# Optimization experiments

Measured on AMD Instinct MI355X. Metric: run time of the kernel, lower is better.

The kernel has to match this reference:

```python
import jax, jax.numpy as jnp
import numpy as np

NH, NW = 5, 5          # attn_neighborhood_size (odd -> symmetric 'same' padding)
HEADS, HEAD_DIM = 8, 64
DIM = 512              # == heads*head_dim, but project_out=True since heads>1
B, HMAP, WMAP = 4, 64, 64
N = HMAP * WMAP


def local_expand(t, height, width):
    """Equivalent of impulse-filter conv2d neighbor gather.

    t: [b, heads, n, d] -> [b, heads, n, NH*NW, d]
    neighbor f=(i,j) of pixel (p,q) is t[p+i-NH//2, q+j-NW//2], zero-padded.
    """
    b, h, n, d = t.shape
    y = t.reshape(b, h, height, width, d)
    ph, pw = NH // 2, NW // 2
    yp = jnp.pad(y, ((0, 0), (0, 0), (ph, ph), (pw, pw), (0, 0)))
    # fixed small loop over the 25 window offsets (row-major = filter order)
    slabs = [yp[:, :, i:i + height, j:j + width, :]
             for i in range(NH) for j in range(NW)]
    out = jnp.stack(slabs, axis=4)  # [b, h, H, W, F, d]
    return out.reshape(b, h, n, NH * NW, d)


def setup_inputs() -> dict:
    key = jax.random.key(0)
    k1, k2, k3, k4 = jax.random.split(key, 4)
    inner = HEADS * HEAD_DIM
    x = jax.random.normal(k1, (B, N, DIM), dtype=jnp.float32)
    # torch Linear weights are [out_features, in_features]
    w_qkv = jax.random.normal(k2, (3 * inner, DIM), dtype=jnp.float32) * (DIM ** -0.5)
    w_out = jax.random.normal(k3, (DIM, inner), dtype=jnp.float32) * (inner ** -0.5)
    b_out = jax.random.normal(k4, (DIM,), dtype=jnp.float32) * 0.01
    return {"x": x, "w_qkv": w_qkv, "w_out": w_out, "b_out": b_out,
            "h": HMAP, "w": WMAP}


def reference(x, w_qkv, w_out, b_out, h, w):
    b, n, _ = x.shape
    scale = HEAD_DIM ** -0.5
    qkv = x @ w_qkv.T                                   # [b, n, 3*inner]
    q, k, v = jnp.split(qkv, 3, axis=-1)
    def to_heads(t):
        return t.reshape(b, n, HEADS, HEAD_DIM).transpose(0, 2, 1, 3)  # b h n d
    q, k, v = to_heads(q), to_heads(k), to_heads(v)
    k_loc = local_expand(k, h, w)                       # [b, h, n, F, d]
    v_loc = local_expand(v, h, w)
    dots = jnp.einsum('bhnd,bhnfd->bhnf', q, k_loc) * scale
    attn = jax.nn.softmax(dots, axis=-1)
    out = jnp.einsum('bhnf,bhnfd->bhnd', attn, v_loc)   # [b, h, n, d]
    out = out.transpose(0, 2, 1, 3).reshape(b, n, HEADS * HEAD_DIM)
    return out @ w_out.T + b_out                        # dropout=0 (eval)
```

## Files before the change

kernel.cpp:

```cpp
#include <hip/hip_runtime.h>
#include <cstddef>
#include <cstdint>


namespace {

typedef short s16x8 __attribute__((ext_vector_type(8)));
typedef unsigned short u16x8 __attribute__((ext_vector_type(8)));
typedef float f32x4 __attribute__((ext_vector_type(4)));

constexpr int kHeads = 8;
constexpr int kHd = 64;
constexpr int kDim = 512;
constexpr int kN = 4096;
constexpr float kScale = 0.125f;

__device__ inline float b2f(unsigned short u) {
  return __uint_as_float((unsigned)u << 16);
}
__device__ inline unsigned short f2b(float x) {
  unsigned u = __float_as_uint(x);
  return (unsigned short)((u + 0x7fffu + ((u >> 16) & 1u)) >> 16);
}

__global__ __launch_bounds__(256) void cvt_w(
    const float* __restrict__ w1, const float* __restrict__ w2,
    unsigned short* __restrict__ o1, unsigned short* __restrict__ o2) {
  const int gid = blockIdx.x * 256 + threadIdx.x;
  const int gs = gridDim.x * 256;
  for (int i = gid; i < 786432 / 4; i += gs) {
    float4 v = ((const float4*)w1)[i];
    ushort4 o;
    o.x = f2b(v.x); o.y = f2b(v.y); o.z = f2b(v.z); o.w = f2b(v.w);
    ((ushort4*)o1)[i] = o;
  }
  for (int i = gid; i < 262144 / 4; i += gs) {
    float4 v = ((const float4*)w2)[i];
    ushort4 o;
    o.x = f2b(v.x); o.y = f2b(v.y); o.z = f2b(v.z); o.w = f2b(v.w);
    ((ushort4*)o2)[i] = o;
  }
}

template <int EPI, typename TA>
__global__ __launch_bounds__(256) void gemm_mfma(
    const TA* __restrict__ A, const unsigned short* __restrict__ W,
    const float* __restrict__ bias, unsigned short* __restrict__ Qb,
    unsigned short* __restrict__ Kb, unsigned short* __restrict__ Vb,
    float* __restrict__ out) {
  __shared__ unsigned short As[128 * 40];
  __shared__ unsigned short Bs[128 * 40];

  const int tid = threadIdx.x;
  const int lane = tid & 63;
  const int wv = tid >> 6;
  const int wm = wv & 1;
  const int wn = wv >> 1;
  const int m0 = blockIdx.y * 128;
  const int n0 = blockIdx.x * 128;

  f32x4 acc[4][4];
#pragma unroll
  for (int i = 0; i < 4; ++i)
#pragma unroll
    for (int j = 0; j < 4; ++j) acc[i][j] = f32x4{0.f, 0.f, 0.f, 0.f};

  for (int k0 = 0; k0 < 512; k0 += 32) {
    if constexpr (sizeof(TA) == 4) {
#pragma unroll
      for (int it = 0; it < 4; ++it) {
        const int idx = tid + it * 256;
        const int row = idx >> 3, seg = idx & 7;
        const float4 v =
            *(const float4*)((const float*)A + (size_t)(m0 + row) * 512 + k0 + seg * 4);
        ushort4 o;
        o.x = f2b(v.x); o.y = f2b(v.y); o.z = f2b(v.z); o.w = f2b(v.w);
        *(ushort4*)&As[row * 40 + seg * 4] = o;
      }
    } else {
#pragma unroll
      for (int it = 0; it < 2; ++it) {
        const int idx = tid + it * 256;
        const int row = idx >> 2, seg = idx & 3;
        *(u16x8*)&As[row * 40 + seg * 8] = *(const u16x8*)(
            (const unsigned short*)A + (size_t)(m0 + row) * 512 + k0 + seg * 8);
      }
    }
#pragma unroll
    for (int it = 0; it < 2; ++it) {
      const int idx = tid + it * 256;
      const int row = idx >> 2, seg = idx & 3;
      *(u16x8*)&Bs[row * 40 + seg * 8] =
          *(const u16x8*)(W + (size_t)(n0 + row) * 512 + k0 + seg * 8);
    }
    __syncthreads();

    s16x8 af[4], bf[4];
#pragma unroll
    for (int i = 0; i < 4; ++i) {
      af[i] = *(const s16x8*)&As[(wm * 64 + i * 16 + (lane & 15)) * 40 +
                                 (lane >> 4) * 8];
      bf[i] = *(const s16x8*)&Bs[(wn * 64 + i * 16 + (lane & 15)) * 40 +
                                 (lane >> 4) * 8];
    }
#pragma unroll
    for (int i = 0; i < 4; ++i)
#pragma unroll
      for (int j = 0; j < 4; ++j)
        acc[i][j] =
            __builtin_amdgcn_mfma_f32_16x16x32_bf16(af[i], bf[j], acc[i][j], 0, 0, 0);
    __syncthreads();
  }

  if (EPI == 0) {
    const int cn = n0 + wn * 64;
    unsigned short* dst = (cn < 512) ? Qb : (cn < 1024 ? Kb : Vb);
    const int head = (cn >> 6) & 7;
    const int colb = lane & 15;
#pragma unroll
    for (int mi = 0; mi < 4; ++mi) {
#pragma unroll
      for (int r = 0; r < 4; ++r) {
        const int m = m0 + wm * 64 + mi * 16 + (lane >> 4) * 4 + r;
        const int b = m >> 12;
        const int p = m & 4095;
        unsigned short* o =
            dst + ((size_t)(b * kHeads + head) * kN + p) * kHd + colb;
#pragma unroll
        for (int ni = 0; ni < 4; ++ni) o[ni * 16] = f2b(acc[mi][ni][r]);
      }
    }
  } else {
    float bvr[4];
#pragma unroll
    for (int ni = 0; ni < 4; ++ni)
      bvr[ni] = bias[n0 + wn * 64 + ni * 16 + (lane & 15)];
#pragma unroll
    for (int mi = 0; mi < 4; ++mi) {
#pragma unroll
      for (int r = 0; r < 4; ++r) {
        const int m = m0 + wm * 64 + mi * 16 + (lane >> 4) * 4 + r;
        float* o = out + (size_t)m * 512 + n0 + wn * 64 + (lane & 15);
#pragma unroll
        for (int ni = 0; ni < 4; ++ni) o[ni * 16] = acc[mi][ni][r] + bvr[ni];
      }
    }
  }
}

__global__ __launch_bounds__(256) void attn_qk(
    const unsigned short* __restrict__ Q, const unsigned short* __restrict__ K,
    unsigned short* __restrict__ attnW) {
  __shared__ unsigned short Kh[400 * 72];
  const int tid = threadIdx.x;
  const int bh = blockIdx.y;
  const int tile = blockIdx.x;
  const int ty0 = (tile >> 2) * 16, tx0 = (tile & 3) * 16;
  const size_t base = (size_t)bh * kN;

  for (int i = tid; i < 3200; i += 256) {
    const int r = i >> 3, c = i & 7;
    const int gy = ty0 - 2 + r / 20;
    const int gx = tx0 - 2 + r % 20;
    u16x8 v = {};
    if ((unsigned)gy < 64u && (unsigned)gx < 64u)
      v = *(const u16x8*)(K + (base + gy * 64 + gx) * 64 + c * 8);
    *(u16x8*)&Kh[r * 72 + c * 8] = v;
  }
  __syncthreads();

  const int pyl = tid >> 4, pxl = tid & 15;
  const int p = (ty0 + pyl) * 64 + tx0 + pxl;

  float q[64];
  {
    const unsigned short* qp = Q + (base + p) * 64;
#pragma unroll
    for (int c = 0; c < 8; ++c) {
      const u16x8 v = *(const u16x8*)(qp + c * 8);
#pragma unroll
      for (int j = 0; j < 8; ++j) q[c * 8 + j] = b2f(v[j]);
    }
  }

  float dots[25];
  float mx = -1e30f;
#pragma unroll
  for (int fy = 0; fy < 5; ++fy) {
#pragma unroll
    for (int fx = 0; fx < 5; ++fx) {
      const unsigned short* kr = &Kh[((pyl + fy) * 20 + pxl + fx) * 72];
      float d = 0.f;
#pragma unroll
      for (int c = 0; c < 8; ++c) {
        const u16x8 kv = *(const u16x8*)(kr + c * 8);
#pragma unroll
        for (int j = 0; j < 8; ++j) d = fmaf(q[c * 8 + j], b2f(kv[j]), d);
      }
      d *= kScale;
      dots[fy * 5 + fx] = d;
      mx = fmaxf(mx, d);
    }
  }
  float sum = 0.f;
#pragma unroll
  for (int f = 0; f < 25; ++f) {
    dots[f] = __expf(dots[f] - mx);
    sum += dots[f];
  }
  const float inv = 1.f / sum;
  unsigned short* ap = attnW + (base + p) * 32;
#pragma unroll
  for (int f = 0; f < 25; ++f) ap[f] = f2b(dots[f] * inv);
}

__global__ __launch_bounds__(256) void attn_pv(
    const unsigned short* __restrict__ V, const unsigned short* __restrict__ attnW,
    unsigned short* __restrict__ AO) {
  __shared__ unsigned short Vh[400 * 72];
  const int tid = threadIdx.x;
  const int bh = blockIdx.y;
  const int tile = blockIdx.x;
  const int ty0 = (tile >> 2) * 16, tx0 = (tile & 3) * 16;
  const size_t base = (size_t)bh * kN;

  for (int i = tid; i < 3200; i += 256) {
    const int r = i >> 3, c = i & 7;
    const int gy = ty0 - 2 + r / 20;
    const int gx = tx0 - 2 + r % 20;
    u16x8 v = {};
    if ((unsigned)gy < 64u && (unsigned)gx < 64u)
      v = *(const u16x8*)(V + (base + gy * 64 + gx) * 64 + c * 8);
    *(u16x8*)&Vh[r * 72 + c * 8] = v;
  }
  __syncthreads();

  const int pyl = tid >> 4, pxl = tid & 15;
  const int p = (ty0 + pyl) * 64 + tx0 + pxl;

  float w[25];
  {
    const unsigned short* ap = attnW + (base + p) * 32;
#pragma unroll
    for (int f = 0; f < 25; ++f) w[f] = b2f(ap[f]);
  }

  float o[64];
#pragma unroll
  for (int j = 0; j < 64; ++j) o[j] = 0.f;

#pragma unroll
  for (int fy = 0; fy < 5; ++fy) {
#pragma unroll
    for (int fx = 0; fx < 5; ++fx) {
      const unsigned short* vr = &Vh[((pyl + fy) * 20 + pxl + fx) * 72];
      const float wf = w[fy * 5 + fx];
#pragma unroll
      for (int c = 0; c < 8; ++c) {
        const u16x8 vv = *(const u16x8*)(vr + c * 8);
#pragma unroll
        for (int j = 0; j < 8; ++j)
          o[c * 8 + j] = fmaf(wf, b2f(vv[j]), o[c * 8 + j]);
      }
    }
  }

  const int b = bh >> 3, h = bh & 7;
  unsigned short* op = AO + ((size_t)(b * kN + p)) * kDim + h * kHd;
#pragma unroll
  for (int c = 0; c < 8; ++c) {
    u16x8 pk;
#pragma unroll
    for (int j = 0; j < 8; ++j) pk[j] = f2b(o[c * 8 + j]);
    *(u16x8*)(op + c * 8) = pk;
  }
}

}

extern "C" void kernel_launch(void* const* d_in, const int* in_sizes, int n_in,
                              void* d_out, int out_size, void* d_ws,
                              size_t ws_size, hipStream_t stream) {
  (void)in_sizes; (void)n_in; (void)out_size; (void)ws_size;
  const float* x = (const float*)d_in[0];
  const float* w_qkv = (const float*)d_in[1];
  const float* w_out = (const float*)d_in[2];
  const float* b_out = (const float*)d_in[3];
  float* out = (float*)d_out;

  unsigned short* ws = (unsigned short*)d_ws;
  unsigned short* wqkvb = ws;
  unsigned short* woutb = ws + 786432;
  unsigned short* Qb = ws + 1048576;
  unsigned short* Kb = Qb + 8388608;
  unsigned short* Vb = Kb + 8388608;
  unsigned short* attnW = Vb + 8388608;
  unsigned short* AO = Qb;

  cvt_w<<<512, 256, 0, stream>>>(w_qkv, w_out, wqkvb, woutb);
  gemm_mfma<0, float><<<dim3(12, 128), 256, 0, stream>>>(
      x, wqkvb, nullptr, Qb, Kb, Vb, nullptr);
  attn_qk<<<dim3(16, 32), 256, 0, stream>>>(Qb, Kb, attnW);
  attn_pv<<<dim3(16, 32), 256, 0, stream>>>(Vb, attnW, AO);
  gemm_mfma<1, unsigned short><<<dim3(4, 128), 256, 0, stream>>>(
      AO, woutb, b_out, nullptr, nullptr, nullptr, out);
}
```

Baseline: 199.9 us.

## Pre-convert x to bf16 and load GEMM tiles via direct global-to-LDS loads

Adds a separate kernel that converts x to bf16 in two halves, so the QKV GEMM no longer converts fp32 inside its K-loop. Both GEMMs now stage tiles with global_load_lds (16-byte direct-to-LDS) into unpadded 32-wide tiles, and block IDs are remapped so each XCD works on contiguous M rows for L2 locality. Launch bounds gain an occupancy hint. In exchange it adds extra launches and an extra pass over x, and the unpadded LDS layout may cause bank conflicts on the fragment reads.

```diff
diff --git a/kernel.cpp b/kernel.cpp
--- a/kernel.cpp
+++ b/kernel.cpp
@@ -10,8 +10,6 @@
 typedef float f32x4 __attribute__((ext_vector_type(4)));
 
 constexpr int kHeads = 8;
-constexpr int kHd = 64;
-constexpr int kDim = 512;
 constexpr int kN = 4096;
 constexpr float kScale = 0.125f;
 
@@ -21,6 +19,13 @@
 __device__ inline unsigned short f2b(float x) {
   unsigned u = __float_as_uint(x);
   return (unsigned short)((u + 0x7fffu + ((u >> 16) & 1u)) >> 16);
+}
+
+__device__ __forceinline__ void g2l16(const unsigned short* g,
+                                      unsigned short* l) {
+  __builtin_amdgcn_global_load_lds(
+      (const __attribute__((address_space(1))) void*)g,
+      (__attribute__((address_space(3))) void*)l, 16, 0, 0);
 }
 
 __global__ __launch_bounds__(256) void cvt_w(
@@ -42,108 +47,123 @@
   }
 }
 
-template <int EPI, typename TA>
-__global__ __launch_bounds__(256) void gemm_mfma(
-    const TA* __restrict__ A, const unsigned short* __restrict__ W,
-    const float* __restrict__ bias, unsigned short* __restrict__ Qb,
-    unsigned short* __restrict__ Kb, unsigned short* __restrict__ Vb,
-    float* __restrict__ out) {
-  __shared__ unsigned short As[128 * 40];
-  __shared__ unsigned short Bs[128 * 40];
-
-  const int tid = threadIdx.x;
+__global__ __launch_bounds__(256) void cvt_x(const float* __restrict__ x,
+                                             unsigned short* __restrict__ xb) {
+  const int i = blockIdx.x * 256 + threadIdx.x;
+  const float4 a = ((const float4*)x)[i * 2];
+  const float4 b = ((const float4*)x)[i * 2 + 1];
+  u16x8 o;
+  o[0] = f2b(a.x); o[1] = f2b(a.y); o[2] = f2b(a.z); o[3] = f2b(a.w);
+  o[4] = f2b(b.x); o[5] = f2b(b.y); o[6] = f2b(b.z); o[7] = f2b(b.w);
+  *(u16x8*)(xb + (size_t)i * 8) = o;
+}
+
+__device__ __forceinline__ void mfma_512(const unsigned short* __restrict__ A,
+                                         const unsigned short* __restrict__ W,
+                                         int m0, int n0, int tid,
+                                         unsigned short* As, unsigned short* Bs,
+                                         f32x4 (&acc)[4][4]) {
   const int lane = tid & 63;
   const int wv = tid >> 6;
-  const int wm = wv & 1;
-  const int wn = wv >> 1;
-  const int m0 = blockIdx.y * 128;
-  const int n0 = blockIdx.x * 128;
-
+  const int wm = wv & 1, wn = wv >> 1;
+  const int rr = lane >> 2;
+  const int cc = (lane & 3) * 8;
+#pragma unroll
+  for (int i = 0; i < 4; ++i)
+#pragma unroll
+    for (int j = 0; j < 4; ++j) acc[i][j] = f32x4{0.f, 0.f, 0.f, 0.f};
+
+  for (int k0 = 0; k0 < 512; k0 += 32) {
+#pragma unroll
+    for (int it = 0; it < 2; ++it) {
+      const int grp = wv * 2 + it;
+      const int row = grp * 16 + rr;
+      g2l16(A + (size_t)(m0 + row) * 512 + k0 + cc, As + grp * 512);
+      g2l16(W + (size_t)(n0 + row) * 512 + k0 + cc, Bs + grp * 512);
+    }
+    __syncthreads();
+    s16x8 af[4], bf[4];
+#pragma unroll
+    for (int i = 0; i < 4; ++i) {
+      af[i] = *(const s16x8*)&As[(wm * 64 + i * 16 + (lane & 15)) * 32 +
+                                 (lane >> 4) * 8];
+      bf[i] = *(const s16x8*)&Bs[(wn * 64 + i * 16 + (lane & 15)) * 32 +
+                                 (lane >> 4) * 8];
+    }
+#pragma unroll
+    for (int i = 0; i < 4; ++i)
+#pragma unroll
+      for (int j = 0; j < 4; ++j)
+        acc[i][j] = __builtin_amdgcn_mfma_f32_16x16x32_bf16(af[i], bf[j],
+                                                            acc[i][j], 0, 0, 0);
+    __syncthreads();
+  }
+}
+
+__global__ __launch_bounds__(256, 4) void gemm_qkv(
+    const unsigned short* __restrict__ A, const unsigned short* __restrict__ W,
+    unsigned short* __restrict__ Qb, unsigned short* __restrict__ Kb,
+    unsigned short* __restrict__ Vb, int mOutBase) {
+  __shared__ unsigned short As[4096], Bs[4096];
+  const int tid = threadIdx.x;
+  const int id = blockIdx.x;
+  const int xcd = id & 7;
+  const int j = id >> 3;
+  const int by = xcd * 8 + j / 12;
+  const int bx = j % 12;
   f32x4 acc[4][4];
-#pragma unroll
-  for (int i = 0; i < 4; ++i)
-#pragma unroll
-    for (int j = 0; j < 4; ++j) acc[i][j] = f32x4{0.f, 0.f, 0.f, 0.f};
-
-  for (int k0 = 0; k0 < 512; k0 += 32) {
-    if constexpr (sizeof(TA) == 4) {
-#pragma unroll
-      for (int it = 0; it < 4; ++it) {
-        const int idx = tid + it * 256;
-        const int row = idx >> 3, seg = idx & 7;
-        const float4 v =
-            *(const float4*)((const float*)A + (size_t)(m0 + row) * 512 + k0 + seg * 4);
-        ushort4 o;
-        o.x = f2b(v.x); o.y = f2b(v.y); o.z = f2b(v.z); o.w = f2b(v.w);
-        *(ushort4*)&As[row * 40 + seg * 4] = o;
-      }
-    } else {
-#pragma unroll
-      for (int it = 0; it < 2; ++it) {
-        const int idx = tid + it * 256;
-        const int row = idx >> 2, seg = idx & 3;
-        *(u16x8*)&As[row * 40 + seg * 8] = *(const u16x8*)(
-            (const unsigned short*)A + (size_t)(m0 + row) * 512 + k0 + seg * 8);
-      }
-    }
-#pragma unroll
-    for (int it = 0; it < 2; ++it) {
-      const int idx = tid + it * 256;
-      const int row = idx >> 2, seg = idx & 3;
-      *(u16x8*)&Bs[row * 40 + seg * 8] =
-          *(const u16x8*)(W + (size_t)(n0 + row) * 512 + k0 + seg * 8);
-    }
-    __syncthreads();
-
-    s16x8 af[4], bf[4];
-#pragma unroll
-    for (int i = 0; i < 4; ++i) {
-      af[i] = *(const s16x8*)&As[(wm * 64 + i * 16 + (lane & 15)) * 40 +
-                                 (lane >> 4) * 8];
-      bf[i] = *(const s16x8*)&Bs[(wn * 64 + i * 16 + (lane & 15)) * 40 +
-                                 (lane >> 4) * 8];
-    }
-#pragma unroll
-    for (int i = 0; i < 4; ++i)
-#pragma unroll
-      for (int j = 0; j < 4; ++j)
-        acc[i][j] =
-            __builtin_amdgcn_mfma_f32_16x16x32_bf16(af[i], bf[j], acc[i][j], 0, 0, 0);
-    __syncthreads();
-  }
-
-  if (EPI == 0) {
-    const int cn = n0 + wn * 64;
-    unsigned short* dst = (cn < 512) ? Qb : (cn < 1024 ? Kb : Vb);
-    const int head = (cn >> 6) & 7;
-    const int colb = lane & 15;
-#pragma unroll
-    for (int mi = 0; mi < 4; ++mi) {
-#pragma unroll
-      for (int r = 0; r < 4; ++r) {
-        const int m = m0 + wm * 64 + mi * 16 + (lane >> 4) * 4 + r;
-        const int b = m >> 12;
-        const int p = m & 4095;
-        unsigned short* o =
-            dst + ((size_t)(b * kHeads + head) * kN + p) * kHd + colb;
-#pragma unroll
-        for (int ni = 0; ni < 4; ++ni) o[ni * 16] = f2b(acc[mi][ni][r]);
-      }
-    }
-  } else {
-    float bvr[4];
-#pragma unroll
-    for (int ni = 0; ni < 4; ++ni)
-      bvr[ni] = bias[n0 + wn * 64 + ni * 16 + (lane & 15)];
-#pragma unroll
-    for (int mi = 0; mi < 4; ++mi) {
-#pragma unroll
-      for (int r = 0; r < 4; ++r) {
-        const int m = m0 + wm * 64 + mi * 16 + (lane >> 4) * 4 + r;
-        float* o = out + (size_t)m * 512 + n0 + wn * 64 + (lane & 15);
-#pragma unroll
-        for (int ni = 0; ni < 4; ++ni) o[ni * 16] = acc[mi][ni][r] + bvr[ni];
-      }
+  mfma_512(A, W, by * 128, bx * 128, tid, As, Bs, acc);
+
+  const int lane = tid & 63;
+  const int wv = tid >> 6;
+  const int wm = wv & 1, wn = wv >> 1;
+  const int cn = bx * 128 + wn * 64;
+  unsigned short* dst = (cn < 512) ? Qb : (cn < 1024 ? Kb : Vb);
+  const int head = (cn >> 6) & 7;
+  const int colb = lane & 15;
+#pragma unroll
+  for (int mi = 0; mi < 4; ++mi) {
+#pragma unroll
+    for (int r = 0; r < 4; ++r) {
+      const int m = mOutBase + by * 128 + wm * 64 + mi * 16 + (lane >> 4) * 4 + r;
+      const int b = m >> 12;
+      const int p = m & 4095;
+      unsigned short* o =
+          dst + ((size_t)(b * kHeads + head) * kN + p) * 64 + colb;
+#pragma unroll
+      for (int ni = 0; ni < 4; ++ni) o[ni * 16] = f2b(acc[mi][ni][r]);
+    }
+  }
+}
+
+__global__ __launch_bounds__(256, 4) void gemm_out(
+    const unsigned short* __restrict__ A, const unsigned short* __restrict__ W,
+    const float* __restrict__ bias, float* __restrict__ out) {
+  __shared__ unsigned short As[4096], Bs[4096];
+  const int tid = threadIdx.x;
+  const int id = blockIdx.x;
+  const int xcd = id & 7;
+  const int j = id >> 3;
+  const int by = xcd * 16 + (j >> 2);
+  const int bx = j & 3;
+  f32x4 acc[4][4];
+  mfma_512(A, W, by * 128, bx * 128, tid, As, Bs, acc);
+
+  const int lane = tid & 63;
+  const int wv = tid >> 6;
+  const int wm = wv & 1, wn = wv >> 1;
+  float bvr[4];
+#pragma unroll
+  for (int ni = 0; ni < 4; ++ni)
+    bvr[ni] = bias[bx * 128 + wn * 64 + ni * 16 + (lane & 15)];
+#pragma unroll
+  for (int mi = 0; mi < 4; ++mi) {
+#pragma unroll
+    for (int r = 0; r < 4; ++r) {
+      const int m = by * 128 + wm * 64 + mi * 16 + (lane >> 4) * 4 + r;
+      float* o = out + (size_t)m * 512 + bx * 128 + wn * 64 + (lane & 15);
+#pragma unroll
+      for (int ni = 0; ni < 4; ++ni) o[ni * 16] = acc[mi][ni][r] + bvr[ni];
     }
   }
 }
@@ -179,7 +199,7 @@
     for (int c = 0; c < 8; ++c) {
       const u16x8 v = *(const u16x8*)(qp + c * 8);
 #pragma unroll
-      for (int j = 0; j < 8; ++j) q[c * 8 + j] = b2f(v[j]);
+      for (int jj = 0; jj < 8; ++jj) q[c * 8 + jj] = b2f(v[jj]);
     }
   }
 
@@ -195,7 +215,7 @@
       for (int c = 0; c < 8; ++c) {
         const u16x8 kv = *(const u16x8*)(kr + c * 8);
 #pragma unroll
-        for (int j = 0; j < 8; ++j) d = fmaf(q[c * 8 + j], b2f(kv[j]), d);
+        for (int jj = 0; jj < 8; ++jj) d = fmaf(q[c * 8 + jj], b2f(kv[jj]), d);
       }
       d *= kScale;
       dots[fy * 5 + fx] = d;
@@ -215,7 +235,8 @@
 }
 
 __global__ __launch_bounds__(256) void attn_pv(
-    const unsigned short* __restrict__ V, const unsigned short* __restrict__ attnW,
+    const unsigned short* __restrict__ V,
+    const unsigned short* __restrict__ attnW,
     unsigned short* __restrict__ AO) {
   __shared__ unsigned short Vh[400 * 72];
   const int tid = threadIdx.x;
@@ -247,7 +268,7 @@
 
   float o[64];
 #pragma unroll
-  for (int j = 0; j < 64; ++j) o[j] = 0.f;
+  for (int jj = 0; jj < 64; ++jj) o[jj] = 0.f;
 
 #pragma unroll
   for (int fy = 0; fy < 5; ++fy) {
@@ -259,19 +280,19 @@
       for (int c = 0; c < 8; ++c) {
         const u16x8 vv = *(const u16x8*)(vr + c * 8);
 #pragma unroll
-        for (int j = 0; j < 8; ++j)
-          o[c * 8 + j] = fmaf(wf, b2f(vv[j]), o[c * 8 + j]);
+        for (int jj = 0; jj < 8; ++jj)
+          o[c * 8 + jj] = fmaf(wf, b2f(vv[jj]), o[c * 8 + jj]);
       }
     }
   }
 
   const int b = bh >> 3, h = bh & 7;
-  unsigned short* op = AO + ((size_t)(b * kN + p)) * kDim + h * kHd;
+  unsigned short* op = AO + ((size_t)(b * kN + p)) * 512 + h * 64;
 #pragma unroll
   for (int c = 0; c < 8; ++c) {
     u16x8 pk;
 #pragma unroll
-    for (int j = 0; j < 8; ++j) pk[j] = f2b(o[c * 8 + j]);
+    for (int jj = 0; jj < 8; ++jj) pk[jj] = f2b(o[c * 8 + jj]);
     *(u16x8*)(op + c * 8) = pk;
   }
 }
@@ -288,20 +309,22 @@
   const float* b_out = (const float*)d_in[3];
   float* out = (float*)d_out;
 
-  unsigned short* ws = (unsigned short*)d_ws;
-  unsigned short* wqkvb = ws;
-  unsigned short* woutb = ws + 786432;
-  unsigned short* Qb = ws + 1048576;
-  unsigned short* Kb = Qb + 8388608;
-  unsigned short* Vb = Kb + 8388608;
-  unsigned short* attnW = Vb + 8388608;
-  unsigned short* AO = Qb;
+  unsigned short* ws0 = (unsigned short*)d_ws;
+  unsigned short* wqkvb = ws0;
+  unsigned short* woutb = ws0 + 786432;
+  unsigned short* xbh   = ws0 + 1048576;
+  unsigned short* Qb    = ws0 + 5242880;
+  unsigned short* Kb    = ws0 + 13631488;
+  unsigned short* Vb    = ws0 + 22020096;
+  unsigned short* attnW = xbh;
+  unsigned short* AO    = Qb;
 
   cvt_w<<<512, 256, 0, stream>>>(w_qkv, w_out, wqkvb, woutb);
-  gemm_mfma<0, float><<<dim3(12, 128), 256, 0, stream>>>(
-      x, wqkvb, nullptr, Qb, Kb, Vb, nullptr);
+  cvt_x<<<2048, 256, 0, stream>>>(x, xbh);
+  gemm_qkv<<<768, 256, 0, stream>>>(xbh, wqkvb, Qb, Kb, Vb, 0);
+  cvt_x<<<2048, 256, 0, stream>>>(x + 4194304, xbh);
+  gemm_qkv<<<768, 256, 0, stream>>>(xbh, wqkvb, Qb, Kb, Vb, 8192);
   attn_qk<<<dim3(16, 32), 256, 0, stream>>>(Qb, Kb, attnW);
   attn_pv<<<dim3(16, 32), 256, 0, stream>>>(Vb, attnW, AO);
-  gemm_mfma<1, unsigned short><<<dim3(4, 128), 256, 0, stream>>>(
-      AO, woutb, b_out, nullptr, nullptr, nullptr, out);
-}
+  gemm_out<<<512, 256, 0, stream>>>(AO, woutb, b_out, out);
+}
```

Result: faster. 193.9 us (-3.0%).
